# Performance work log

Measured on AMD Instinct MI355X. Metric: run time of the kernel, lower is better.

Reference implementation:

```python
import jax, jax.numpy as jnp
import numpy as np

TRAIN_COUNT, FEAT = 20000, 40
BATCH, NN, M = 2048, 64, 10


def _safe_l2(d2):
    # sqrt with zero (not NaN/inf) gradient at d2 == 0 (diagonal of pairwise dists)
    pos = d2 > 0
    return jnp.where(pos, jnp.sqrt(jnp.where(pos, d2, 1.0)), 0.0)


def setup_inputs() -> dict:
    key = jax.random.key(0)
    k1, k2, k3, k4 = jax.random.split(key, 4)
    x = jax.random.normal(k1, (TRAIN_COUNT, FEAT), dtype=jnp.float32)
    batch_indices = jax.random.randint(k2, (BATCH,), 0, TRAIN_COUNT)
    batch_nn_indices = jax.random.randint(k3, (BATCH, NN), 0, TRAIN_COUNT)
    batch_nn_targets = jax.random.normal(k4, (BATCH, NN, M), dtype=jnp.float32)
    length_scale = jnp.ones((M,), dtype=jnp.float32)
    eps = 1e-3 * jnp.ones((M,), dtype=jnp.float32)
    return {
        "x": x,
        "length_scale": length_scale,
        "eps": eps,
        "batch_indices": batch_indices,
        "batch_nn_indices": batch_nn_indices,
        "batch_nn_targets": batch_nn_targets,
    }


def reference(x, length_scale, eps, batch_indices, batch_nn_indices, batch_nn_targets):
    b, nn, m = batch_nn_targets.shape
    xb = x[batch_indices]          # (b, f)
    xn = x[batch_nn_indices]       # (b, nn, f)

    # crosswise l2 distances (b, nn)
    cd = _safe_l2(jnp.sum((xb[:, None, :] - xn) ** 2, axis=-1))
    # pairwise l2 distances (b, nn, nn)
    pd = _safe_l2(jnp.sum((xn[:, :, None, :] - xn[:, None, :, :]) ** 2, axis=-1))

    # Matern nu = 1/2: k(d) = exp(-d / length_scale); vectorized over the m models
    Kcross = jnp.exp(-cd[None, :, :] / length_scale[:, None, None])            # (m, b, nn)
    K = jnp.exp(-pd[None, :, :, :] / length_scale[:, None, None, None])        # (m, b, nn, nn)
    eye = jnp.eye(nn, dtype=K.dtype)
    Kp = K + eps[:, None, None, None] * eye                                     # homoscedastic perturb

    Y = jnp.moveaxis(batch_nn_targets, -1, 0)[..., None]                        # (m, b, nn, 1)
    F = jnp.linalg.solve(Kp, Y)[..., 0]                                         # (m, b, nn)
    predictions = jnp.einsum("mbn,mbn->bm", Kcross, F)

    G = jnp.linalg.solve(Kp, Kcross[..., None])[..., 0]                         # (m, b, nn)
    variances = 1.0 - jnp.einsum("mbn,mbn->bm", Kcross, G)

    sigma_sq = jnp.sum(Y[..., 0] * F, axis=(1, 2)) / (b * nn)                   # (m,)
    return predictions, variances, sigma_sq
```

## Files before the change

### kernel.cpp

```cpp
#include <hip/hip_runtime.h>
#include <math.h>

#define BATCH 2048
#define NN 64
#define FEAT 40
#define M 10
#define ASZ (NN * NN + 130)

typedef float v2f __attribute__((ext_vector_type(2)));

#define PKFMA_SV(acc, s_src, v_src) \
    asm("v_pk_fma_f32 %0, %1, %2, %0" : "+v"(acc) : "s"(s_src), "v"(v_src))
#define PKFMA_VV(acc, a_src, b_src) \
    asm("v_pk_fma_f32 %0, %1, %2, %0" : "+v"(acc) : "v"(a_src), "v"(b_src))

__device__ __forceinline__ float rl(float v, int l) {
    return __int_as_float(__builtin_amdgcn_readlane(__float_as_int(v), l));
}
__device__ __forceinline__ int rli(int v, int l) {
    return __builtin_amdgcn_readlane(v, l);
}
__device__ __forceinline__ float wsum(float v) {
#pragma unroll
    for (int o = 32; o >= 1; o >>= 1) v += __shfl_xor(v, o, 64);
    return v;
}

__global__ __launch_bounds__(64)
__attribute__((amdgpu_waves_per_eu(2, 2)))
void muygps_kernel(
    const float* __restrict__ x,
    const float* __restrict__ ls,
    const float* __restrict__ epsv,
    const int*   __restrict__ bidx,
    const int*   __restrict__ nidx,
    const float* __restrict__ tgt,
    float* __restrict__ out,
    float* __restrict__ ws)
{
    __shared__ float A[ASZ];
    __shared__ float rvb[NN];

    const int b    = blockIdx.x;
    const int lane = threadIdx.x;

    const int nv = nidx[b * NN + lane];
    const float* xr0 = x + (size_t)nv * FEAT;
    v2f xc2[FEAT / 2];
#pragma unroll
    for (int q = 0; q < FEAT / 4; ++q) {
        const float4 v = *(const float4*)(xr0 + 4 * q);
        xc2[2 * q]     = v2f{v.x, v.y};
        xc2[2 * q + 1] = v2f{v.z, v.w};
    }
    v2f nl2 = {0.f, 0.f};
#pragma unroll
    for (int q = 0; q < FEAT / 2; ++q) PKFMA_VV(nl2, xc2[q], xc2[q]);
    const float nl = nl2.x + nl2.y;

    const v2f* xbv = (const v2f*)(x + (size_t)bidx[b] * FEAT);
    v2f gc2 = {0.f, 0.f}, nb2 = {0.f, 0.f};
#pragma unroll
    for (int q = 0; q < FEAT / 2; ++q) {
        const v2f xbq = xbv[q];
        PKFMA_VV(gc2, xbq, xc2[q]);
        PKFMA_VV(nb2, xbq, xbq);
    }
    float cd2 = ((nb2.x + nb2.y) + nl) - 2.f * (gc2.x + gc2.y);
    cd2 = (cd2 < 0.05f) ? 0.f : cd2;
    const float cdv = sqrtf(cd2);

    unsigned done = 0;
    const unsigned all = (1u << M) - 1u;
    while (true) {
        const int   lead = __ffs(~done) - 1;
        const float lls  = ls[lead];
        const float lep  = epsv[lead];
        const float il   = -1.0f / lls;

        for (int i = 0; i < NN; i += 2) {
            const int ri0 = rli(nv, i), ri1 = rli(nv, i + 1);
            const v2f* rp0 = (const v2f*)(x + (size_t)ri0 * FEAT);
            const v2f* rp1 = (const v2f*)(x + (size_t)ri1 * FEAT);
            v2f g0 = {0.f, 0.f}, g1 = {0.f, 0.f};
#pragma unroll
            for (int q = 0; q < FEAT / 2; ++q) {
                const v2f r0q = rp0[q], r1q = rp1[q];
                PKFMA_SV(g0, r0q, xc2[q]);
                PKFMA_SV(g1, r1q, xc2[q]);
            }
            const float ga = g0.x + g0.y, gb = g1.x + g1.y;
            float d2a = (rl(ga, i) + nl) - 2.f * ga;
            float d2b = (rl(gb, i + 1) + nl) - 2.f * gb;
            d2a = (d2a < 0.05f) ? 0.f : d2a;
            d2b = (d2b < 0.05f) ? 0.f : d2b;
            float va = __expf(sqrtf(d2a) * il);
            float vb = __expf(sqrtf(d2b) * il);
            if (lane == i)     va += lep;
            if (lane == i + 1) vb += lep;
            A[i * NN + lane]       = va;
            A[(i + 1) * NN + lane] = vb;
        }
        const float kcv = __expf(cdv * il);

        float z[M + 1];
        z[0] = kcv;
        {
            const float* trow = tgt + ((size_t)b * NN + lane) * M;
#pragma unroll
            for (int q = 0; q < M / 2; ++q) {
                const float2 v = *(const float2*)(trow + 2 * q);
                z[2 * q + 1] = v.x; z[2 * q + 2] = v.y;
            }
        }

        float pc0 = A[lane];
        float pc1 = A[NN + lane];
        for (int p = 0; p < 31; ++p) {
            const int k = 2 * p;
            const float d0  = rl(pc0, 0);
            const float r0  = __builtin_amdgcn_rcpf(d0);
            const float cv0 = pc0 * (-r0);
            pc1 = fmaf(cv0, rl(pc0, 1), pc1);
            const float d1  = rl(pc1, 1);
            const float r1  = __builtin_amdgcn_rcpf(d1);
            const float cv1 = pc1 * (-r1);
            A[k * NN + k + lane]      = (lane >= 1) ? pc0 * r0 : 0.f;
            A[k * NN + NN + k + lane] = (lane >= 2) ? pc1 * r1 : 0.f;
            rvb[k]     = r0;
            rvb[k + 1] = r1;
            float t2 = A[(k + 2) * NN + k + lane];
            float t3 = A[(k + 3) * NN + k + lane];
            t2 = fmaf(cv0, rl(pc0, 2), t2); t2 = fmaf(cv1, rl(pc1, 2), t2);
            t3 = fmaf(cv0, rl(pc0, 3), t3); t3 = fmaf(cv1, rl(pc1, 3), t3);
            const float n0 = __shfl_down(t2, 2, 64);
            const float n1 = __shfl_down(t3, 2, 64);
            for (int i = k + 4; i < NN; ++i) {
                const float l0 = rl(pc0, i - k);
                const float l1 = rl(pc1, i - k);
                float t = A[i * NN + k + lane];
                t = fmaf(cv0, l0, t);
                t = fmaf(cv1, l1, t);
                A[i * NN + k + lane] = t;
            }
            pc0 = n0; pc1 = n1;
        }
        {
            const int k = 62;
            const float d0  = rl(pc0, 0);
            const float r0  = __builtin_amdgcn_rcpf(d0);
            const float cv0 = pc0 * (-r0);
            pc1 = fmaf(cv0, rl(pc0, 1), pc1);
            const float d1  = rl(pc1, 1);
            const float r1  = __builtin_amdgcn_rcpf(d1);
            A[k * NN + k + lane]      = (lane >= 1) ? pc0 * r0 : 0.f;
            A[k * NN + NN + k + lane] = (lane >= 2) ? pc1 * r1 : 0.f;
            rvb[k]     = r0;
            rvb[k + 1] = r1;
        }

        for (int k = 0; k < NN - 1; ++k) {
            float lv = A[k * NN + lane];
            lv = (lane > k) ? -lv : 0.f;
#pragma unroll
            for (int j = 0; j < M + 1; ++j) {
                const float s = rl(z[j], k);
                z[j] = fmaf(lv, s, z[j]);
            }
        }

        const float rvv = rvb[lane];
        const float zc  = z[0];
        const float quad = wsum(zc * zc * rvv);
        unsigned newly = 0;
#pragma unroll
        for (int m = 0; m < M; ++m) {
            if (!(done & (1u << m)) && ls[m] == lls && epsv[m] == lep) {
                const float zm = z[m + 1];
                const float pm = wsum(zc * zm * rvv);
                const float sm = wsum(zm * zm * rvv);
                if (lane == 0) {
                    out[b * M + m] = pm;
                    out[BATCH * M + b * M + m] = 1.0f - quad;
                    ws[m * BATCH + b] = sm;
                }
                newly |= 1u << m;
            }
        }
        done |= newly;
        if (done == all) break;
    }
}

__global__ __launch_bounds__(640)
void sigma_reduce(const float* __restrict__ ws, float* __restrict__ out) {
    const int w = threadIdx.x >> 6, lane = threadIdx.x & 63;
    const float4* p = (const float4*)(ws + w * BATCH);
    float a = 0.f;
#pragma unroll
    for (int i = 0; i < BATCH / 4 / 64; ++i) {
        const float4 v = p[i * 64 + lane];
        a += (v.x + v.y) + (v.z + v.w);
    }
    a = wsum(a);
    if (lane == 0)
        out[2 * BATCH * M + w] = a * (1.0f / (float)(BATCH * NN));
}

extern "C" void kernel_launch(void* const* d_in, const int* in_sizes, int n_in,
                              void* d_out, int out_size, void* d_ws, size_t ws_size,
                              hipStream_t stream) {
    const float* x   = (const float*)d_in[0];
    const float* lsp = (const float*)d_in[1];
    const float* ep  = (const float*)d_in[2];
    const int*   bi  = (const int*)d_in[3];
    const int*   ni  = (const int*)d_in[4];
    const float* tg  = (const float*)d_in[5];
    float* out = (float*)d_out;
    float* ws  = (float*)d_ws;

    muygps_kernel<<<BATCH, 64, 0, stream>>>(x, lsp, ep, bi, ni, tg, out, ws);
    sigma_reduce<<<1, 640, 0, stream>>>(ws, out);
}
```

Before: 156.0 us.

## Store Cholesky rows unshifted, prefetch LDS rows, and coalesce output writes

```diff
diff --git a/kernel.cpp b/kernel.cpp
--- a/kernel.cpp
+++ b/kernel.cpp
@@ -5,7 +5,7 @@
 #define NN 64
 #define FEAT 40
 #define M 10
-#define ASZ (NN * NN + 130)
+#define ASZ (NN * NN + 64)
 
 typedef float v2f __attribute__((ext_vector_type(2)));
 
@@ -78,6 +78,7 @@
         const float lep  = epsv[lead];
         const float il   = -1.0f / lls;
 
+#pragma unroll 2
         for (int i = 0; i < NN; i += 2) {
             const int ri0 = rli(nv, i), ri1 = rli(nv, i + 1);
             const v2f* rp0 = (const v2f*)(x + (size_t)ri0 * FEAT);
@@ -118,76 +119,84 @@
         float pc1 = A[NN + lane];
         for (int p = 0; p < 31; ++p) {
             const int k = 2 * p;
-            const float d0  = rl(pc0, 0);
+            const float d0  = rl(pc0, k);
             const float r0  = __builtin_amdgcn_rcpf(d0);
             const float cv0 = pc0 * (-r0);
-            pc1 = fmaf(cv0, rl(pc0, 1), pc1);
-            const float d1  = rl(pc1, 1);
+            pc1 = fmaf(cv0, rl(pc0, k + 1), pc1);
+            const float d1  = rl(pc1, k + 1);
             const float r1  = __builtin_amdgcn_rcpf(d1);
             const float cv1 = pc1 * (-r1);
-            A[k * NN + k + lane]      = (lane >= 1) ? pc0 * r0 : 0.f;
-            A[k * NN + NN + k + lane] = (lane >= 2) ? pc1 * r1 : 0.f;
+            A[k * NN + lane]      = (lane > k)     ? pc0 * r0 : 0.f;
+            A[k * NN + NN + lane] = (lane > k + 1) ? pc1 * r1 : 0.f;
             rvb[k]     = r0;
             rvb[k + 1] = r1;
-            float t2 = A[(k + 2) * NN + k + lane];
-            float t3 = A[(k + 3) * NN + k + lane];
-            t2 = fmaf(cv0, rl(pc0, 2), t2); t2 = fmaf(cv1, rl(pc1, 2), t2);
-            t3 = fmaf(cv0, rl(pc0, 3), t3); t3 = fmaf(cv1, rl(pc1, 3), t3);
-            const float n0 = __shfl_down(t2, 2, 64);
-            const float n1 = __shfl_down(t3, 2, 64);
-            for (int i = k + 4; i < NN; ++i) {
-                const float l0 = rl(pc0, i - k);
-                const float l1 = rl(pc1, i - k);
-                float t = A[i * NN + k + lane];
-                t = fmaf(cv0, l0, t);
-                t = fmaf(cv1, l1, t);
-                A[i * NN + k + lane] = t;
-            }
-            pc0 = n0; pc1 = n1;
+            float t2 = A[(k + 2) * NN + lane];
+            float t3 = A[(k + 3) * NN + lane];
+            float u0 = 0.f, u1 = 0.f;
+            if (k + 4 < NN) { u0 = A[(k + 4) * NN + lane]; u1 = A[(k + 5) * NN + lane]; }
+            t2 = fmaf(cv0, rl(pc0, k + 2), t2); t2 = fmaf(cv1, rl(pc1, k + 2), t2);
+            t3 = fmaf(cv0, rl(pc0, k + 3), t3); t3 = fmaf(cv1, rl(pc1, k + 3), t3);
+            for (int i = k + 4; i < NN; i += 2) {
+                float a0 = u0, a1 = u1;
+                if (i + 2 < NN) {
+                    u0 = A[(i + 2) * NN + lane];
+                    u1 = A[(i + 3) * NN + lane];
+                }
+                a0 = fmaf(cv0, rl(pc0, i), a0);     a0 = fmaf(cv1, rl(pc1, i), a0);
+                a1 = fmaf(cv0, rl(pc0, i + 1), a1); a1 = fmaf(cv1, rl(pc1, i + 1), a1);
+                A[i * NN + lane]       = a0;
+                A[(i + 1) * NN + lane] = a1;
+            }
+            pc0 = t2; pc1 = t3;
         }
         {
-            const int k = 62;
-            const float d0  = rl(pc0, 0);
+            const float d0  = rl(pc0, 62);
             const float r0  = __builtin_amdgcn_rcpf(d0);
             const float cv0 = pc0 * (-r0);
-            pc1 = fmaf(cv0, rl(pc0, 1), pc1);
-            const float d1  = rl(pc1, 1);
+            pc1 = fmaf(cv0, rl(pc0, 63), pc1);
+            const float d1  = rl(pc1, 63);
             const float r1  = __builtin_amdgcn_rcpf(d1);
-            A[k * NN + k + lane]      = (lane >= 1) ? pc0 * r0 : 0.f;
-            A[k * NN + NN + k + lane] = (lane >= 2) ? pc1 * r1 : 0.f;
-            rvb[k]     = r0;
-            rvb[k + 1] = r1;
-        }
-
+            A[62 * NN + lane] = (lane > 62) ? pc0 * r0 : 0.f;
+            rvb[62] = r0;
+            rvb[63] = r1;
+        }
+
+        float lr = A[lane];
         for (int k = 0; k < NN - 1; ++k) {
-            float lv = A[k * NN + lane];
-            lv = (lane > k) ? -lv : 0.f;
+            const float lrn = A[(k + 1) * NN + lane];
+            const float lv = -lr;
 #pragma unroll
             for (int j = 0; j < M + 1; ++j) {
                 const float s = rl(z[j], k);
                 z[j] = fmaf(lv, s, z[j]);
             }
+            lr = lrn;
         }
 
         const float rvv = rvb[lane];
         const float zc  = z[0];
         const float quad = wsum(zc * zc * rvv);
-        unsigned newly = 0;
+        unsigned mb = 0;
+#pragma unroll
+        for (int m = 0; m < M; ++m)
+            if (!(done & (1u << m)) && ls[m] == lls && epsv[m] == lep)
+                mb |= 1u << m;
+        float predv = 0.f, sigv = 0.f;
 #pragma unroll
         for (int m = 0; m < M; ++m) {
-            if (!(done & (1u << m)) && ls[m] == lls && epsv[m] == lep) {
+            if (mb & (1u << m)) {
                 const float zm = z[m + 1];
                 const float pm = wsum(zc * zm * rvv);
                 const float sm = wsum(zm * zm * rvv);
-                if (lane == 0) {
-                    out[b * M + m] = pm;
-                    out[BATCH * M + b * M + m] = 1.0f - quad;
-                    ws[m * BATCH + b] = sm;
-                }
-                newly |= 1u << m;
-            }
-        }
-        done |= newly;
+                if (lane == m) { predv = pm; sigv = sm; }
+            }
+        }
+        if (lane < M && ((mb >> lane) & 1u)) {
+            out[b * M + lane] = predv;
+            out[BATCH * M + b * M + lane] = 1.0f - quad;
+            ws[lane * BATCH + b] = sigv;
+        }
+        done |= mb;
         if (done == all) break;
     }
 }
```

After: 156.6 us. No clear change (+0.4%).
